# Kernel optimization log

Measured on AMD Instinct MI355X. Metric: run time of the kernel, lower is better.

The kernel has to match this reference:

```python
import jax, jax.numpy as jnp
import numpy as np

B, H, S, D = 2, 16, 2048, 128

def setup_inputs() -> dict:
    key = jax.random.key(0)
    kq, kk, kv = jax.random.split(key, 3)
    Q = jax.random.normal(kq, (B, H, S, D), dtype=jnp.float32)
    K = jax.random.normal(kk, (B, H, S, D), dtype=jnp.float32)
    V = jax.random.normal(kv, (B, H, S, D), dtype=jnp.float32)
    return {"Q": Q, "K": K, "V": V}

def reference(Q, K, V):
    # FlashAttentionV3 forward: scaled dot-product attention with causal mask,
    # scale defaults to 1/sqrt(head_dim), dropout=0.
    head_dim = Q.shape[-1]
    scale = 1.0 / jnp.sqrt(jnp.asarray(head_dim, dtype=Q.dtype))
    # scores: [B, H, S, S]
    scores = jnp.einsum('bhqd,bhkd->bhqk', Q, K) * scale
    seq_q, seq_k = Q.shape[2], K.shape[2]
    causal_mask = jnp.tril(jnp.ones((seq_q, seq_k), dtype=bool))  # [S, S]
    scores = jnp.where(causal_mask, scores, jnp.asarray(-jnp.inf, dtype=scores.dtype))
    attn = jax.nn.softmax(scores, axis=-1)
    out = jnp.einsum('bhqk,bhkd->bhqd', attn, V)
    return out
```

## Files before the change

kernel.cpp:

```cpp
#include <hip/hip_runtime.h>
#include <hip/hip_bf16.h>

typedef __attribute__((ext_vector_type(8))) short short8;
typedef __attribute__((ext_vector_type(4))) float f32x4;
typedef __attribute__((ext_vector_type(4))) unsigned int u32x4;

#define S_LEN 2048
#define D_DIM 128
#define NT 32
#define NQT 16
#define TILE_FRAG_BYTES 16384u
#define VF_OFF ((size_t)32 * NT * TILE_FRAG_BYTES)

__device__ __forceinline__ unsigned short bfbits(float f) {
  return __builtin_bit_cast(unsigned short, __float2bfloat16(f));
}
__device__ __forceinline__ unsigned int pk2(float lo, float hi) {
  return (unsigned int)bfbits(lo) | ((unsigned int)bfbits(hi) << 16);
}
__device__ __forceinline__ float exp2f_hw(float x) {
  float r;
  asm("v_exp_f32 %0, %1" : "=v"(r) : "v"(x));
  return r;
}
__device__ __forceinline__ void gload16(const void* g, void* l) {
  __builtin_amdgcn_global_load_lds(
      (const __attribute__((address_space(1))) unsigned int*)g,
      (__attribute__((address_space(3))) unsigned int*)l, 16, 0, 0);
}

extern "C" __global__ void __launch_bounds__(256)
fa_prepass_kernel(const float* __restrict__ Kg, const float* __restrict__ Vg,
                  char* __restrict__ ws)
{
  const unsigned gid = blockIdx.x * 256 + threadIdx.x;
  const unsigned g = gid & ((1u << 20) - 1);
  const int ln = g & 63, l15 = ln & 15, lhi = (ln >> 4) & 3;
  const int f  = (g >> 6) & 15;
  const int t  = (g >> 10) & 31;
  const int bh = g >> 15;
  char* dst = ws + ((size_t)(bh * NT + t) * 16 + f) * 1024 + ln * 16;
  if (gid < (1u << 20)) {
    const int c = f >> 2, kk = f & 3;
    const int row = t * 64 + ((l15 >> 2) << 3) + (l15 & 3) + ((c & 1) << 2) + ((c >> 1) << 5);
    const float* src = Kg + (size_t)bh * S_LEN * D_DIM + (size_t)row * D_DIM + kk * 32 + lhi * 8;
    f32x4 a = *(const f32x4*)src;
    f32x4 b = *(const f32x4*)(src + 4);
    u32x4 u;
    u[0] = pk2(a[0], a[1]); u[1] = pk2(a[2], a[3]);
    u[2] = pk2(b[0], b[1]); u[3] = pk2(b[2], b[3]);
    *(u32x4*)dst = u;
  } else {
    const int dc = f >> 1, w = f & 1;
    const float* src = Vg + (size_t)bh * S_LEN * D_DIM
                     + (size_t)(t * 64 + w * 32 + lhi * 8) * D_DIM + dc * 16 + l15;
    float v[8];
    #pragma unroll
    for (int j = 0; j < 8; ++j) v[j] = src[(size_t)j * D_DIM];
    u32x4 u;
    u[0] = pk2(v[0], v[1]); u[1] = pk2(v[2], v[3]);
    u[2] = pk2(v[4], v[5]); u[3] = pk2(v[6], v[7]);
    *(u32x4*)(dst + VF_OFF) = u;
  }
}

extern "C" __global__ void __launch_bounds__(256, 2)
fa_fwd_kernel(const float* __restrict__ Qg, const char* __restrict__ ws,
              float* __restrict__ Og)
{
  __shared__ __align__(16) char smem[2][16384];

  const int bh = blockIdx.x;
  const int by = (int)blockIdx.y;
  const int qt = (by < 8) ? (15 - 2 * by) : (2 * (by - 8));
  const int m0 = qt * 128;
  const int tid = threadIdx.x;
  const int wv  = tid >> 6;
  const int ln  = tid & 63;
  const int l15 = ln & 15;
  const int lhi = ln >> 4;

  const float* Qb = Qg + (size_t)bh * S_LEN * D_DIM;
  float*       Ob = Og + (size_t)bh * S_LEN * D_DIM;
  const char*  kfb = ws + (size_t)bh * NT * TILE_FRAG_BYTES;
  const char*  vfbg = kfb + VF_OFF;
  const int    voff = ln * 16;

  const float scale = 0.12753102f;
  const int wrow_lo = m0 + wv * 32;

  short8 qf[2][4];
  #pragma unroll
  for (int g = 0; g < 2; ++g) {
    const float* qsrc = Qb + (size_t)(wrow_lo + g * 16 + l15) * D_DIM + lhi * 8;
    #pragma unroll
    for (int kk = 0; kk < 4; ++kk) {
      f32x4 a = *(const f32x4*)(qsrc + kk * 32);
      f32x4 b = *(const f32x4*)(qsrc + kk * 32 + 4);
      u32x4 u;
      u[0] = pk2(a[0] * scale, a[1] * scale);
      u[1] = pk2(a[2] * scale, a[3] * scale);
      u[2] = pk2(b[0] * scale, b[1] * scale);
      u[3] = pk2(b[2] * scale, b[3] * scale);
      qf[g][kk] = __builtin_bit_cast(short8, u);
    }
  }

  auto stage_k = [&](int t, char* buf) {
    const char* kt = kfb + (size_t)t * TILE_FRAG_BYTES;
    #pragma unroll
    for (int i = 0; i < 4; ++i) {
      const int fi = wv * 4 + i;
      gload16(kt + (size_t)fi * 1024 + voff, buf + fi * 1024);
    }
  };

  const f32x4 fzero = {0.f, 0.f, 0.f, 0.f};
  f32x4 oacc[2][8];
  #pragma unroll
  for (int g = 0; g < 2; ++g)
    #pragma unroll
    for (int i = 0; i < 8; ++i) oacc[g][i] = fzero;
  float m_run[2] = {8.0f, 8.0f};
  float l_run[2] = {0.f, 0.f};

  const int ntiles = 2 * qt + 2;

  stage_k(0, smem[0]);
  __syncthreads();

  int cur = 0;
  for (int t = 0; t < ntiles; ++t) {
    const int kv0 = t * 64;
    const bool comp = (kv0 <= wrow_lo + 31);
    if (t + 1 < ntiles) stage_k(t + 1, smem[cur ^ 1]);

    if (comp) {
      const char* kt = smem[cur];
      const char* vg = vfbg + (size_t)t * TILE_FRAG_BYTES;

      f32x4 sacc[2][4];
      __builtin_amdgcn_s_setprio(1);
      #pragma unroll
      for (int c = 0; c < 4; ++c) {
        sacc[0][c] = fzero; sacc[1][c] = fzero;
        #pragma unroll
        for (int kk = 0; kk < 4; ++kk) {
          short8 kf = *(const short8*)(kt + (c * 4 + kk) * 1024 + voff);
          sacc[0][c] = __builtin_amdgcn_mfma_f32_16x16x32_bf16(kf, qf[0][kk], sacc[0][c], 0, 0, 0);
          sacc[1][c] = __builtin_amdgcn_mfma_f32_16x16x32_bf16(kf, qf[1][kk], sacc[1][c], 0, 0, 0);
        }
      }
      __builtin_amdgcn_s_setprio(0);

      short8 vfA[8];
      #pragma unroll
      for (int i = 0; i < 8; ++i)
        vfA[i] = *(const short8*)(vg + i * 1024 + voff);

      if (kv0 + 63 > wrow_lo) {
        #pragma unroll
        for (int g = 0; g < 2; ++g) {
          const int qg = wrow_lo + g * 16 + l15;
          #pragma unroll
          for (int c = 0; c < 4; ++c) {
            const int kvb = kv0 + (c >> 1) * 32 + (c & 1) * 4 + lhi * 8;
            #pragma unroll
            for (int r = 0; r < 4; ++r)
              if (kvb + r > qg) sacc[g][c][r] = -INFINITY;
          }
        }
      }

      float mt[2];
      #pragma unroll
      for (int g = 0; g < 2; ++g) {
        float mA[4];
        #pragma unroll
        for (int r = 0; r < 4; ++r)
          mA[r] = fmaxf(fmaxf(sacc[g][0][r], sacc[g][1][r]),
                        fmaxf(sacc[g][2][r], sacc[g][3][r]));
        mt[g] = fmaxf(fmaxf(mA[0], mA[1]), fmaxf(mA[2], mA[3]));
        #pragma unroll
        for (int c = 0; c < 4; ++c)
          #pragma unroll
          for (int r = 0; r < 4; ++r)
            sacc[g][c][r] = exp2f_hw(sacc[g][c][r] - m_run[g]);
      }
      #pragma unroll
      for (int g = 0; g < 2; ++g) {
        float m = fmaxf(mt[g], __shfl_xor(mt[g], 16));
        m = fmaxf(m, __shfl_xor(m, 32));
        if (!__all(m <= m_run[g] + 11.5f)) {
          const float m_new = fmaxf(m_run[g], m);
          const float al = exp2f_hw(m_run[g] - m_new);
          #pragma unroll
          for (int c = 0; c < 4; ++c)
            #pragma unroll
            for (int r = 0; r < 4; ++r) sacc[g][c][r] *= al;
          #pragma unroll
          for (int dc = 0; dc < 8; ++dc)
            #pragma unroll
            for (int r = 0; r < 4; ++r) oacc[g][dc][r] *= al;
          l_run[g] *= al;
          m_run[g] = m_new;
        }
        float sA[4];
        #pragma unroll
        for (int r = 0; r < 4; ++r)
          sA[r] = (sacc[g][0][r] + sacc[g][1][r]) + (sacc[g][2][r] + sacc[g][3][r]);
        float rs = (sA[0] + sA[1]) + (sA[2] + sA[3]);
        rs += __shfl_xor(rs, 16);
        rs += __shfl_xor(rs, 32);
        l_run[g] += rs;
      }

      short8 pfrag[2][2];
      #pragma unroll
      for (int g = 0; g < 2; ++g)
        #pragma unroll
        for (int w = 0; w < 2; ++w) {
          u32x4 u;
          u[0] = pk2(sacc[g][2 * w][0], sacc[g][2 * w][1]);
          u[1] = pk2(sacc[g][2 * w][2], sacc[g][2 * w][3]);
          u[2] = pk2(sacc[g][2 * w + 1][0], sacc[g][2 * w + 1][1]);
          u[3] = pk2(sacc[g][2 * w + 1][2], sacc[g][2 * w + 1][3]);
          pfrag[g][w] = __builtin_bit_cast(short8, u);
        }

      short8 vfB[8];
      #pragma unroll
      for (int i = 0; i < 8; ++i)
        vfB[i] = *(const short8*)(vg + (8 + i) * 1024 + voff);

      __builtin_amdgcn_s_setprio(1);
      #pragma unroll
      for (int dc = 0; dc < 4; ++dc)
        #pragma unroll
        for (int w = 0; w < 2; ++w) {
          oacc[0][dc] = __builtin_amdgcn_mfma_f32_16x16x32_bf16(vfA[dc * 2 + w], pfrag[0][w], oacc[0][dc], 0, 0, 0);
          oacc[1][dc] = __builtin_amdgcn_mfma_f32_16x16x32_bf16(vfA[dc * 2 + w], pfrag[1][w], oacc[1][dc], 0, 0, 0);
        }
      #pragma unroll
      for (int dc = 4; dc < 8; ++dc)
        #pragma unroll
        for (int w = 0; w < 2; ++w) {
          oacc[0][dc] = __builtin_amdgcn_mfma_f32_16x16x32_bf16(vfB[(dc - 4) * 2 + w], pfrag[0][w], oacc[0][dc], 0, 0, 0);
          oacc[1][dc] = __builtin_amdgcn_mfma_f32_16x16x32_bf16(vfB[(dc - 4) * 2 + w], pfrag[1][w], oacc[1][dc], 0, 0, 0);
        }
      __builtin_amdgcn_s_setprio(0);
    }

    __syncthreads();
    cur ^= 1;
  }

  #pragma unroll
  for (int g = 0; g < 2; ++g) {
    const float invl = 1.0f / l_run[g];
    float* orow = Ob + (size_t)(wrow_lo + g * 16 + l15) * D_DIM + lhi * 4;
    #pragma unroll
    for (int dc = 0; dc < 8; ++dc) {
      f32x4 o;
      #pragma unroll
      for (int r = 0; r < 4; ++r) o[r] = oacc[g][dc][r] * invl;
      *(f32x4*)(orow + dc * 16) = o;
    }
  }
}

extern "C" void kernel_launch(void* const* d_in, const int* in_sizes, int n_in,
                              void* d_out, int out_size, void* d_ws, size_t ws_size,
                              hipStream_t stream) {
  const float* Q = (const float*)d_in[0];
  const float* K = (const float*)d_in[1];
  const float* V = (const float*)d_in[2];
  float* O = (float*)d_out;
  char* ws = (char*)d_ws;
  fa_prepass_kernel<<<dim3(8192), dim3(256), 0, stream>>>(K, V, ws);
  dim3 grid(32 , NQT);
  fa_fwd_kernel<<<grid, dim3(256), 0, stream>>>(Q, ws, O);
}
```

Baseline: 86.89 us.

## Shrink query tile to 64 rows with 2-wave blocks and 32 q-tiles

Halves the query tile per block (two waves, 64 rows) and doubles the grid's q-tile count, so each block processes only the KV tiles up to its own diagonal with no per-wave skip logic. Each wave now stages eight K fragments per tile, and all sixteen V fragments are loaded up front. The causal mask is applied only on the final tile, and q-tiles are reordered to pair heavy and light blocks for load balance. In exchange, every K tile is loaded twice as often across blocks and per-block overhead grows.

```diff
diff --git a/kernel.cpp b/kernel.cpp
--- a/kernel.cpp
+++ b/kernel.cpp
@@ -8,7 +8,7 @@
 #define S_LEN 2048
 #define D_DIM 128
 #define NT 32
-#define NQT 16
+#define NQT 32
 #define TILE_FRAG_BYTES 16384u
 #define VF_OFF ((size_t)32 * NT * TILE_FRAG_BYTES)
 
@@ -64,7 +64,7 @@
   }
 }
 
-extern "C" __global__ void __launch_bounds__(256, 2)
+extern "C" __global__ void __launch_bounds__(128, 2)
 fa_fwd_kernel(const float* __restrict__ Qg, const char* __restrict__ ws,
               float* __restrict__ Og)
 {
@@ -72,8 +72,11 @@
 
   const int bh = blockIdx.x;
   const int by = (int)blockIdx.y;
-  const int qt = (by < 8) ? (15 - 2 * by) : (2 * (by - 8));
-  const int m0 = qt * 128;
+  int qt;
+  if      (by <  8) qt = 31 - by;
+  else if (by < 16) qt = by - 8;
+  else if (by < 24) qt = 39 - by;
+  else              qt = by - 16;
   const int tid = threadIdx.x;
   const int wv  = tid >> 6;
   const int ln  = tid & 63;
@@ -87,7 +90,7 @@
   const int    voff = ln * 16;
 
   const float scale = 0.12753102f;
-  const int wrow_lo = m0 + wv * 32;
+  const int wrow_lo = qt * 64 + wv * 32;
 
   short8 qf[2][4];
   #pragma unroll
@@ -109,8 +112,8 @@
   auto stage_k = [&](int t, char* buf) {
     const char* kt = kfb + (size_t)t * TILE_FRAG_BYTES;
     #pragma unroll
-    for (int i = 0; i < 4; ++i) {
-      const int fi = wv * 4 + i;
+    for (int i = 0; i < 8; ++i) {
+      const int fi = wv * 8 + i;
       gload16(kt + (size_t)fi * 1024 + voff, buf + fi * 1024);
     }
   };
@@ -124,132 +127,116 @@
   float m_run[2] = {8.0f, 8.0f};
   float l_run[2] = {0.f, 0.f};
 
-  const int ntiles = 2 * qt + 2;
+  const int ntiles = qt + 1;
 
   stage_k(0, smem[0]);
   __syncthreads();
 
   int cur = 0;
   for (int t = 0; t < ntiles; ++t) {
-    const int kv0 = t * 64;
-    const bool comp = (kv0 <= wrow_lo + 31);
     if (t + 1 < ntiles) stage_k(t + 1, smem[cur ^ 1]);
 
-    if (comp) {
-      const char* kt = smem[cur];
-      const char* vg = vfbg + (size_t)t * TILE_FRAG_BYTES;
-
-      f32x4 sacc[2][4];
-      __builtin_amdgcn_s_setprio(1);
-      #pragma unroll
-      for (int c = 0; c < 4; ++c) {
-        sacc[0][c] = fzero; sacc[1][c] = fzero;
-        #pragma unroll
-        for (int kk = 0; kk < 4; ++kk) {
-          short8 kf = *(const short8*)(kt + (c * 4 + kk) * 1024 + voff);
-          sacc[0][c] = __builtin_amdgcn_mfma_f32_16x16x32_bf16(kf, qf[0][kk], sacc[0][c], 0, 0, 0);
-          sacc[1][c] = __builtin_amdgcn_mfma_f32_16x16x32_bf16(kf, qf[1][kk], sacc[1][c], 0, 0, 0);
+    const char* vg = vfbg + (size_t)t * TILE_FRAG_BYTES;
+    short8 vf[16];
+    #pragma unroll
+    for (int i = 0; i < 16; ++i)
+      vf[i] = *(const short8*)(vg + i * 1024 + voff);
+
+    const char* kt = smem[cur];
+
+    f32x4 sacc[2][4];
+    __builtin_amdgcn_s_setprio(1);
+    #pragma unroll
+    for (int c = 0; c < 4; ++c) {
+      sacc[0][c] = fzero; sacc[1][c] = fzero;
+      #pragma unroll
+      for (int kk = 0; kk < 4; ++kk) {
+        short8 kf = *(const short8*)(kt + (c * 4 + kk) * 1024 + voff);
+        sacc[0][c] = __builtin_amdgcn_mfma_f32_16x16x32_bf16(kf, qf[0][kk], sacc[0][c], 0, 0, 0);
+        sacc[1][c] = __builtin_amdgcn_mfma_f32_16x16x32_bf16(kf, qf[1][kk], sacc[1][c], 0, 0, 0);
+      }
+    }
+    __builtin_amdgcn_s_setprio(0);
+
+    if (t == ntiles - 1) {
+      #pragma unroll
+      for (int g = 0; g < 2; ++g) {
+        const int qg = wrow_lo + g * 16 + l15;
+        #pragma unroll
+        for (int c = 0; c < 4; ++c) {
+          const int kvb = t * 64 + (c >> 1) * 32 + (c & 1) * 4 + lhi * 8;
+          #pragma unroll
+          for (int r = 0; r < 4; ++r)
+            if (kvb + r > qg) sacc[g][c][r] = -INFINITY;
         }
       }
-      __builtin_amdgcn_s_setprio(0);
-
-      short8 vfA[8];
-      #pragma unroll
-      for (int i = 0; i < 8; ++i)
-        vfA[i] = *(const short8*)(vg + i * 1024 + voff);
-
-      if (kv0 + 63 > wrow_lo) {
-        #pragma unroll
-        for (int g = 0; g < 2; ++g) {
-          const int qg = wrow_lo + g * 16 + l15;
-          #pragma unroll
-          for (int c = 0; c < 4; ++c) {
-            const int kvb = kv0 + (c >> 1) * 32 + (c & 1) * 4 + lhi * 8;
-            #pragma unroll
-            for (int r = 0; r < 4; ++r)
-              if (kvb + r > qg) sacc[g][c][r] = -INFINITY;
-          }
-        }
-      }
-
-      float mt[2];
-      #pragma unroll
-      for (int g = 0; g < 2; ++g) {
-        float mA[4];
+    }
+
+    float mt[2];
+    #pragma unroll
+    for (int g = 0; g < 2; ++g) {
+      float mA[4];
+      #pragma unroll
+      for (int r = 0; r < 4; ++r)
+        mA[r] = fmaxf(fmaxf(sacc[g][0][r], sacc[g][1][r]),
+                      fmaxf(sacc[g][2][r], sacc[g][3][r]));
+      mt[g] = fmaxf(fmaxf(mA[0], mA[1]), fmaxf(mA[2], mA[3]));
+      #pragma unroll
+      for (int c = 0; c < 4; ++c)
         #pragma unroll
         for (int r = 0; r < 4; ++r)
-          mA[r] = fmaxf(fmaxf(sacc[g][0][r], sacc[g][1][r]),
-                        fmaxf(sacc[g][2][r], sacc[g][3][r]));
-        mt[g] = fmaxf(fmaxf(mA[0], mA[1]), fmaxf(mA[2], mA[3]));
+          sacc[g][c][r] = exp2f_hw(sacc[g][c][r] - m_run[g]);
+    }
+    #pragma unroll
+    for (int g = 0; g < 2; ++g) {
+      float m = fmaxf(mt[g], __shfl_xor(mt[g], 16));
+      m = fmaxf(m, __shfl_xor(m, 32));
+      if (!__all(m <= m_run[g] + 11.5f)) {
+        const float m_new = fmaxf(m_run[g], m);
+        const float al = exp2f_hw(m_run[g] - m_new);
         #pragma unroll
         for (int c = 0; c < 4; ++c)
           #pragma unroll
-          for (int r = 0; r < 4; ++r)
-            sacc[g][c][r] = exp2f_hw(sacc[g][c][r] - m_run[g]);
-      }
-      #pragma unroll
-      for (int g = 0; g < 2; ++g) {
-        float m = fmaxf(mt[g], __shfl_xor(mt[g], 16));
-        m = fmaxf(m, __shfl_xor(m, 32));
-        if (!__all(m <= m_run[g] + 11.5f)) {
-          const float m_new = fmaxf(m_run[g], m);
-          const float al = exp2f_hw(m_run[g] - m_new);
+          for (int r = 0; r < 4; ++r) sacc[g][c][r] *= al;
+        #pragma unroll
+        for (int dc = 0; dc < 8; ++dc)
           #pragma unroll
-          for (int c = 0; c < 4; ++c)
-            #pragma unroll
-            for (int r = 0; r < 4; ++r) sacc[g][c][r] *= al;
-          #pragma unroll
-          for (int dc = 0; dc < 8; ++dc)
-            #pragma unroll
-            for (int r = 0; r < 4; ++r) oacc[g][dc][r] *= al;
-          l_run[g] *= al;
-          m_run[g] = m_new;
-        }
-        float sA[4];
-        #pragma unroll
-        for (int r = 0; r < 4; ++r)
-          sA[r] = (sacc[g][0][r] + sacc[g][1][r]) + (sacc[g][2][r] + sacc[g][3][r]);
-        float rs = (sA[0] + sA[1]) + (sA[2] + sA[3]);
-        rs += __shfl_xor(rs, 16);
-        rs += __shfl_xor(rs, 32);
-        l_run[g] += rs;
-      }
-
-      short8 pfrag[2][2];
-      #pragma unroll
-      for (int g = 0; g < 2; ++g)
-        #pragma unroll
-        for (int w = 0; w < 2; ++w) {
-          u32x4 u;
-          u[0] = pk2(sacc[g][2 * w][0], sacc[g][2 * w][1]);
-          u[1] = pk2(sacc[g][2 * w][2], sacc[g][2 * w][3]);
-          u[2] = pk2(sacc[g][2 * w + 1][0], sacc[g][2 * w + 1][1]);
-          u[3] = pk2(sacc[g][2 * w + 1][2], sacc[g][2 * w + 1][3]);
-          pfrag[g][w] = __builtin_bit_cast(short8, u);
-        }
-
-      short8 vfB[8];
-      #pragma unroll
-      for (int i = 0; i < 8; ++i)
-        vfB[i] = *(const short8*)(vg + (8 + i) * 1024 + voff);
-
-      __builtin_amdgcn_s_setprio(1);
-      #pragma unroll
-      for (int dc = 0; dc < 4; ++dc)
-        #pragma unroll
-        for (int w = 0; w < 2; ++w) {
-          oacc[0][dc] = __builtin_amdgcn_mfma_f32_16x16x32_bf16(vfA[dc * 2 + w], pfrag[0][w], oacc[0][dc], 0, 0, 0);
-          oacc[1][dc] = __builtin_amdgcn_mfma_f32_16x16x32_bf16(vfA[dc * 2 + w], pfrag[1][w], oacc[1][dc], 0, 0, 0);
-        }
-      #pragma unroll
-      for (int dc = 4; dc < 8; ++dc)
-        #pragma unroll
-        for (int w = 0; w < 2; ++w) {
-          oacc[0][dc] = __builtin_amdgcn_mfma_f32_16x16x32_bf16(vfB[(dc - 4) * 2 + w], pfrag[0][w], oacc[0][dc], 0, 0, 0);
-          oacc[1][dc] = __builtin_amdgcn_mfma_f32_16x16x32_bf16(vfB[(dc - 4) * 2 + w], pfrag[1][w], oacc[1][dc], 0, 0, 0);
-        }
-      __builtin_amdgcn_s_setprio(0);
-    }
+          for (int r = 0; r < 4; ++r) oacc[g][dc][r] *= al;
+        l_run[g] *= al;
+        m_run[g] = m_new;
+      }
+      float sA[4];
+      #pragma unroll
+      for (int r = 0; r < 4; ++r)
+        sA[r] = (sacc[g][0][r] + sacc[g][1][r]) + (sacc[g][2][r] + sacc[g][3][r]);
+      float rs = (sA[0] + sA[1]) + (sA[2] + sA[3]);
+      rs += __shfl_xor(rs, 16);
+      rs += __shfl_xor(rs, 32);
+      l_run[g] += rs;
+    }
+
+    short8 pfrag[2][2];
+    #pragma unroll
+    for (int g = 0; g < 2; ++g)
+      #pragma unroll
+      for (int w = 0; w < 2; ++w) {
+        u32x4 u;
+        u[0] = pk2(sacc[g][2 * w][0], sacc[g][2 * w][1]);
+        u[1] = pk2(sacc[g][2 * w][2], sacc[g][2 * w][3]);
+        u[2] = pk2(sacc[g][2 * w + 1][0], sacc[g][2 * w + 1][1]);
+        u[3] = pk2(sacc[g][2 * w + 1][2], sacc[g][2 * w + 1][3]);
+        pfrag[g][w] = __builtin_bit_cast(short8, u);
+      }
+
+    __builtin_amdgcn_s_setprio(1);
+    #pragma unroll
+    for (int dc = 0; dc < 8; ++dc)
+      #pragma unroll
+      for (int w = 0; w < 2; ++w) {
+        oacc[0][dc] = __builtin_amdgcn_mfma_f32_16x16x32_bf16(vf[dc * 2 + w], pfrag[0][w], oacc[0][dc], 0, 0, 0);
+        oacc[1][dc] = __builtin_amdgcn_mfma_f32_16x16x32_bf16(vf[dc * 2 + w], pfrag[1][w], oacc[1][dc], 0, 0, 0);
+      }
+    __builtin_amdgcn_s_setprio(0);
 
     __syncthreads();
     cur ^= 1;
@@ -279,5 +266,5 @@
   char* ws = (char*)d_ws;
   fa_prepass_kernel<<<dim3(8192), dim3(256), 0, stream>>>(K, V, ws);
   dim3 grid(32 , NQT);
-  fa_fwd_kernel<<<grid, dim3(256), 0, stream>>>(Q, ws, O);
-}
+  fa_fwd_kernel<<<grid, dim3(128), 0, stream>>>(Q, ws, O);
+}
```

Measured after the change: 87.03 us. About the same (+0.2%).
